# Optimization experiments

Measured on AMD Instinct MI355X. Metric: run time of the kernel, lower is better.

## Reference

```python
import jax, jax.numpy as jnp
import numpy as np

MAX_DEPTH = 11  # node positions < 2**11 = 2048


def setup_inputs() -> dict:
    key = jax.random.key(0)
    k1, k2, k3, k4, k5 = jax.random.split(key, 5)
    B, S, dim = 4, 1024, 64
    token_types = jax.random.randint(k1, (B, S), 0, 5).astype(jnp.int32)
    # token_values in [-1, 2]: -1 marks out-of-scope for scope tokens;
    # bop uses tv+1 (0..3), nop uses tv+5 (4..7) -- all in-range for the 11-row table
    token_values = (jax.random.randint(k2, (B, S), 0, 4) - 1).astype(jnp.int32)
    node_positions = jax.random.randint(k3, (B, S), 0, 2048).astype(jnp.int32)
    embed_table = jax.random.normal(k4, (11, dim), dtype=jnp.float32)
    # mirrors torch.rand(2,dim,dim).softmax(-1).cumsum(-1) init
    primitives_raw = jnp.cumsum(
        jax.nn.softmax(jax.random.uniform(k5, (2, dim, dim), dtype=jnp.float32), axis=-1),
        axis=-1)
    return {
        "token_types": token_types,
        "token_values": token_values,
        "node_positions": node_positions,
        "embed_table": embed_table,
        "primitives_raw": primitives_raw,
    }


def _forward(token_types, token_values, node_positions, embed_table, primitives_raw):
    dim = embed_table.shape[1]
    B, S = token_types.shape

    # primitives = expm(P - P^H) for each of the 2 generators
    herm = primitives_raw - jnp.swapaxes(primitives_raw, -1, -2)
    prims = jax.vmap(jax.scipy.linalg.expm)(herm)  # [2, dim, dim]

    # --- positional encodings via binary-path matrix products ---
    # path(pos) applies prims[pos%2], then prims[(pos//2)%2], ... until pos==1.
    # Equivalent to the original's per-unique-position masked-linear loop,
    # evaluated per token (== positional_encodings[inverse]).
    maps = jnp.broadcast_to(jnp.eye(dim, dtype=embed_table.dtype), (B, S, dim, dim))
    pos = node_positions
    for _ in range(MAX_DEPTH):
        active = pos > 1
        bit = (pos & 1).astype(jnp.int32)
        step_p = prims[bit]  # [B, S, dim, dim] gather of the per-step generator
        # linear(maps, prim) == maps @ prim.T, applied rowwise to each map matrix
        stepped = jnp.einsum('bsij,bskj->bsik', maps, step_p)
        maps = jnp.where(active[..., None, None], stepped, maps)
        pos = pos >> 1

    # --- content embeddings via masked gathers ---
    tt, tv = token_types, token_values
    sos = tt == 0
    bop = tt == 1
    nop = tt == 2
    scope = tt == 3
    oos = scope & (tv == -1)
    db = tt == 4
    idx = jnp.where(sos, 0,
          jnp.where(bop, tv + 1,
          jnp.where(nop, tv + 5,
          jnp.where(db, 8,
          jnp.where(oos, 10, 0)))))
    valid = sos | bop | nop | db | oos  # in-scope scope tokens stay zero
    content = jnp.where(valid[..., None], embed_table[idx], jnp.zeros((), embed_table.dtype))
    return content, maps


def reference(token_types, token_values, node_positions, embed_table, primitives_raw):
    return _forward(token_types, token_values, node_positions, embed_table, primitives_raw)
```

## Files before the change

kernel.cpp:

```cpp
#include <hip/hip_runtime.h>
#include <hip/hip_bf16.h>
#include <stdint.h>

typedef __attribute__((ext_vector_type(4))) float fx4;
typedef __attribute__((ext_vector_type(16))) float fx16;
typedef __attribute__((ext_vector_type(8))) short bx8;
typedef unsigned short u16;
typedef unsigned int u32;

#define LDW 72
#define PL (64 * LDW)
#define MAGIC 0x9E3779B9u


__device__ __forceinline__ u16 f2bf(float x) {
    u32 u = __float_as_uint(x);
    return (u16)((u + 0x7FFFu + ((u >> 16) & 1u)) >> 16);
}
__device__ __forceinline__ float bf2f(u16 h) { return __uint_as_float(((u32)h) << 16); }

__device__ __forceinline__ bx8 ld32(const u16* p, int band, int kc, int l) {
    return *(const bx8*)(p + (band * 32 + (l & 31)) * LDW + kc * 16 + (l >> 5) * 8);
}

__device__ __forceinline__ void mmG1(const u16* z1h, const u16* z1l,
                                     const u16* z2h, const u16* z2l,
                                     int ti, int tj, int l, fx16& acc) {
    fx16 ca, cb, cc;
#pragma unroll
    for (int i = 0; i < 16; ++i) { ca[i] = 0.f; cb[i] = 0.f; cc[i] = 0.f; }
#pragma unroll
    for (int kc = 0; kc < 4; ++kc) {
        bx8 ah = ld32(z1h, ti, kc, l), al = ld32(z1l, ti, kc, l);
        bx8 bh = ld32(z2h, tj, kc, l), bl = ld32(z2l, tj, kc, l);
        ca = __builtin_amdgcn_mfma_f32_32x32x16_bf16(ah, bh, ca, 0, 0, 0);
        cb = __builtin_amdgcn_mfma_f32_32x32x16_bf16(ah, bl, cb, 0, 0, 0);
        cc = __builtin_amdgcn_mfma_f32_32x32x16_bf16(al, bh, cc, 0, 0, 0);
    }
#pragma unroll
    for (int i = 0; i < 16; ++i) acc[i] = ca[i] + (cb[i] + cc[i]);
}

__device__ __forceinline__ void mmG2(const u16* z1h, const u16* z1l,
                                     const u16* z2h, const u16* z2l,
                                     int ti, int tj, int l, fx16& acc) {
    fx16 ca, cb, cc;
#pragma unroll
    for (int i = 0; i < 16; ++i) { ca[i] = 0.f; cb[i] = 0.f; cc[i] = 0.f; }
#pragma unroll
    for (int kc = 0; kc < 4; ++kc) {
        bx8 ah = ld32(z1h, ti, kc, l), al = ld32(z1l, ti, kc, l);
        bx8 bh = ld32(z2h, tj, kc, l), bl = ld32(z2l, tj, kc, l);
        ca = __builtin_amdgcn_mfma_f32_32x32x16_bf16(bh, ah, ca, 0, 0, 0);
        cb = __builtin_amdgcn_mfma_f32_32x32x16_bf16(bh, al, cb, 0, 0, 0);
        cc = __builtin_amdgcn_mfma_f32_32x32x16_bf16(bl, ah, cc, 0, 0, 0);
    }
#pragma unroll
    for (int i = 0; i < 16; ++i) acc[i] = ca[i] + (cb[i] + cc[i]);
}

__device__ __forceinline__ void stP(u16* hi, u16* lo, int TI, int TJ, int l, const fx16& a) {
    const int Ar = TJ * 32 + (l & 31);
    const int c0 = TI * 32 + 4 * (l >> 5);
#pragma unroll
    for (int q = 0; q < 4; ++q) {
        union { u16 u[4]; uint2 v; } H, L;
#pragma unroll
        for (int r = 0; r < 4; ++r) {
            float v = a[4 * q + r];
            u32 u = __float_as_uint(v);
            H.u[r] = (u16)(u >> 16);
            L.u[r] = f2bf(v - __uint_as_float(u & 0xFFFF0000u));
        }
        *(uint2*)(hi + Ar * LDW + c0 + q * 8) = H.v;
        *(uint2*)(lo + Ar * LDW + c0 + q * 8) = L.v;
    }
}

__device__ __forceinline__ void stG(u16* T, int TI, int TJ, int l, const fx16& a) {
    const int Ar = TJ * 32 + (l & 31);
    const int c0 = TI * 32 + 4 * (l >> 5);
#pragma unroll
    for (int q = 0; q < 4; ++q) {
        union { u16 u[4]; uint2 v; } pk;
#pragma unroll
        for (int r = 0; r < 4; ++r) pk.u[r] = f2bf(a[4 * q + r]);
        *(uint2*)(T + Ar * 64 + c0 + q * 8) = pk.v;
    }
}

__global__ __launch_bounds__(512) void tables_kernel(const float* __restrict__ praw,
                                                     u16* __restrict__ wsP,
                                                     u16* __restrict__ rm_bf,
                                                     u16* __restrict__ cm_bf,
                                                     u32* __restrict__ flags)
{
    __shared__ u16 S[14 * PL];
    __shared__ float Mf[64 * 65];
    const int p = blockIdx.x, tid = threadIdx.x;
    const int w = tid >> 6, l = tid & 63;
    const int wid = w & 3, half = w >> 2;
    const int ti = wid & 1, tj = wid >> 1;

    if (p < 2) {
        const int g = p;
        const float* P = praw + g * 4096;
        u16* p0h = S;            u16* p0l = S + PL;
        u16* p1h = S + 2 * PL;   u16* p1l = S + 3 * PL;
        u16* p2h = S + 4 * PL;   u16* p2l = S + 5 * PL;
        u16* p3h = S + 6 * PL;   u16* p3l = S + 7 * PL;
        float* Mf2 = (float*)(S + 8 * PL);

        const float c0c = 1.0f, c1c = 1.0f, c2c = 0.5f;
        const float c3c = 1.666666666666667e-1f, c4c = 4.166666666666667e-2f;
        const float c5c = 8.333333333333333e-3f, c6c = 1.388888888888889e-3f;
        const float c7c = 1.984126984126984e-4f, c8c = 2.48015873015873e-5f;
        const float c9c = 2.75573192239859e-6f;

        for (int s = tid; s < 4096; s += 512) {
            const int r = s >> 6, c = s & 63;
            const float m = (P[r * 64 + c] - P[c * 64 + r]) * 0.0625f;
            Mf[r * 65 + c] = m;
            u32 um = __float_as_uint(m);
            float lof = m - __uint_as_float(um & 0xFFFF0000u);
            u16 hh = (u16)(um >> 16), ll = f2bf(lof);
            p0h[r * LDW + c] = hh;  p0l[r * LDW + c] = ll;
            p1h[c * LDW + r] = hh;  p1l[c * LDW + r] = ll;
        }
        __syncthreads();

        fx16 acc, v;
        const int gcb = tj * 32 + (l & 31);
        const int r0b = ti * 32 + 4 * (l >> 5);

        if (half == 0) {
            mmG1(p1h, p1l, p0h, p0l, ti, tj, l, acc);
            stP(p2h, p2l, ti, tj, l, acc);
#pragma unroll
            for (int q = 0; q < 4; ++q)
#pragma unroll
                for (int rr = 0; rr < 4; ++rr)
                    Mf2[(r0b + q * 8 + rr) * 65 + gcb] = acc[4 * q + rr];
        }
        __syncthreads();

        if (half == 0) {
            mmG1(p2h, p2l, p0h, p0l, ti, tj, l, acc);
            stP(p3h, p3l, ti, tj, l, acc);
#pragma unroll
            for (int q = 0; q < 4; ++q)
#pragma unroll
                for (int rr = 0; rr < 4; ++rr) {
                    const int gr = r0b + q * 8 + rr;
                    v[4 * q + rr] = c9c * acc[4 * q + rr] + c8c * Mf2[gr * 65 + gcb]
                                  - c7c * Mf[gr * 65 + gcb] + (gr == gcb ? c6c : 0.f);
                }
            stP(p1h, p1l, ti, tj, l, v);
        }
        __syncthreads();

        if (half == 0) {
            mmG1(p3h, p3l, p1h, p1l, ti, tj, l, acc);
#pragma unroll
            for (int q = 0; q < 4; ++q)
#pragma unroll
                for (int rr = 0; rr < 4; ++rr) {
                    const int gr = r0b + q * 8 + rr;
                    v[4 * q + rr] = -acc[4 * q + rr] + c5c * Mf2[gr * 65 + gcb]
                                  - c4c * Mf[gr * 65 + gcb] + (gr == gcb ? c3c : 0.f);
                }
            stP(p0h, p0l, ti, tj, l, v);
        }
        __syncthreads();

        if (half == 0) {
            mmG1(p3h, p3l, p0h, p0l, ti, tj, l, acc);
#pragma unroll
            for (int q = 0; q < 4; ++q)
#pragma unroll
                for (int rr = 0; rr < 4; ++rr) {
                    const int gr = r0b + q * 8 + rr;
                    v[4 * q + rr] = -acc[4 * q + rr] + c2c * Mf2[gr * 65 + gcb]
                                  - c1c * Mf[gr * 65 + gcb] + (gr == gcb ? c0c : 0.f);
                }
            stP(p1h, p1l, ti, tj, l, v);
        } else {
            mmG1(p0h, p0l, p3h, p3l, ti, tj, l, acc);
#pragma unroll
            for (int q = 0; q < 4; ++q)
#pragma unroll
                for (int rr = 0; rr < 4; ++rr) {
                    const int gr = r0b + q * 8 + rr;
                    v[4 * q + rr] = -acc[4 * q + rr] + c2c * Mf2[gr * 65 + gcb]
                                  + c1c * Mf[gr * 65 + gcb] + (gr == gcb ? c0c : 0.f);
                }
            stP(p2h, p2l, ti, tj, l, v);
        }
        __syncthreads();

        u16 *Ych = p2h, *Ycl = p2l, *Xch = p1h, *Xcl = p1l;
        u16 *Ynh = p3h, *Ynl = p3l, *Xnh = p0h, *Xnl = p0l;
#pragma unroll 1
        for (int s4 = 0; s4 < 4; ++s4) {
            if (half == 0) {
                mmG1(Ych, Ycl, Xch, Xcl, ti, tj, l, acc);
                stP(Xnh, Xnl, ti, tj, l, acc);
            } else {
                mmG2(Ych, Ycl, Xch, Xcl, ti, tj, l, acc);
                stP(Ynh, Ynl, tj, ti, l, acc);
            }
            __syncthreads();
            u16* t;
            t = Xch; Xch = Xnh; Xnh = t;   t = Xcl; Xcl = Xnl; Xnl = t;
            t = Ych; Ych = Ynh; Ynh = t;   t = Ycl; Ycl = Ynl; Ynl = t;
        }

        {
            const int base = tid * 8, r = base >> 6, c = base & 63;
            u16* dst = wsP + g * 16384;
            *(uint4*)(dst + base)         = *(const uint4*)(Ych + r * LDW + c);
            *(uint4*)(dst + 4096 + base)  = *(const uint4*)(Ycl + r * LDW + c);
            *(uint4*)(dst + 8192 + base)  = *(const uint4*)(Xch + r * LDW + c);
            *(uint4*)(dst + 12288 + base) = *(const uint4*)(Xcl + r * LDW + c);
        }
        __threadfence();
        __syncthreads();
        if (tid < 64) atomicExch(&flags[(g * 64 + tid) * 32], MAGIC);

        for (int s = tid; s < 4096; s += 512) {
            u16 vv = ((s >> 6) == (s & 63)) ? (u16)0x3F80 : (u16)0;
            rm_bf[p * 4096 + s] = vv;
            cm_bf[p * 4096 + s] = vv;
        }
        return;
    }

    if (tid == 0) {
        while (atomicOr(&flags[(0 * 64 + p) * 32], 0u) != MAGIC) __builtin_amdgcn_s_sleep(8);
        while (atomicOr(&flags[(1 * 64 + p) * 32], 0u) != MAGIC) __builtin_amdgcn_s_sleep(8);
    }
    __syncthreads();
    __threadfence();

    const int d = 31 - __clz(p);

    if (d == 1) {
        const u16* src = wsP + (p & 1) * 16384;
        for (int s = tid; s < 4096; s += 512) {
            rm_bf[p * 4096 + s] = f2bf(bf2f(src[s]) + bf2f(src[4096 + s]));
            cm_bf[p * 4096 + s] = f2bf(bf2f(src[8192 + s]) + bf2f(src[12288 + s]));
        }
        return;
    }

    {
        const int base = tid * 8, r = base >> 6, c = base & 63;
        const int off = r * LDW + c;
        *(uint4*)(S + 0 * PL + off) = *(const uint4*)(wsP + base);
        *(uint4*)(S + 1 * PL + off) = *(const uint4*)(wsP + 4096 + base);
        *(uint4*)(S + 2 * PL + off) = *(const uint4*)(wsP + 8192 + base);
        *(uint4*)(S + 3 * PL + off) = *(const uint4*)(wsP + 12288 + base);
        *(uint4*)(S + 4 * PL + off) = *(const uint4*)(wsP + 16384 + base);
        *(uint4*)(S + 5 * PL + off) = *(const uint4*)(wsP + 16384 + 4096 + base);
        *(uint4*)(S + 6 * PL + off) = *(const uint4*)(wsP + 16384 + 8192 + base);
        *(uint4*)(S + 7 * PL + off) = *(const uint4*)(wsP + 16384 + 12288 + base);
    }
    __syncthreads();

    const int b0 = p & 1, b1 = (p >> 1) & 1, b2 = (p >> 2) & 1, b3 = (p >> 3) & 1,
              b4 = (p >> 4) & 1;
    const u16 *rm0h = S + b0 * 4 * PL,          *rm0l = rm0h + PL;
    const u16 *cm1h = S + b1 * 4 * PL + 2 * PL, *cm1l = cm1h + PL;
    const u16 *rm2h = S + b2 * 4 * PL,          *rm2l = rm2h + PL;
    const u16 *cm3h = S + b3 * 4 * PL + 2 * PL, *cm3l = cm3h + PL;
    u16 *PAh = S + 8 * PL,  *PAl = S + 9 * PL;
    u16 *PBh = S + 10 * PL, *PBl = S + 11 * PL;
    u16 *PCh = S + 12 * PL, *PCl = S + 13 * PL;

    fx16 acc;
    const u16 *fz1h, *fz1l, *fz2h, *fz2l;

    if (d == 2) {
        fz1h = cm1h; fz1l = cm1l; fz2h = rm0h; fz2l = rm0l;
    } else if (d == 3) {
        if (half == 0) {
            mmG1(cm1h, cm1l, rm0h, rm0l, ti, tj, l, acc);
            stP(PAh, PAl, ti, tj, l, acc);
        }
        __syncthreads();
        const u16* c2h = S + b2 * 4 * PL + 2 * PL;
        fz1h = c2h; fz1l = c2h + PL; fz2h = PAh; fz2l = PAl;
    } else {
        if (half == 0) {
            mmG1(cm1h, cm1l, rm0h, rm0l, ti, tj, l, acc);
            stP(PAh, PAl, ti, tj, l, acc);
        } else {
            mmG2(cm3h, cm3l, rm2h, rm2l, ti, tj, l, acc);
            stP(PBh, PBl, tj, ti, l, acc);
        }
        __syncthreads();
        if (d == 4) {
            fz1h = PBh; fz1l = PBl; fz2h = PAh; fz2l = PAl;
        } else {
            if (half == 0) {
                mmG1(PBh, PBl, PAh, PAl, ti, tj, l, acc);
                stP(PCh, PCl, ti, tj, l, acc);
            }
            __syncthreads();
            const u16* c4h = S + b4 * 4 * PL + 2 * PL;
            fz1h = c4h; fz1l = c4h + PL; fz2h = PCh; fz2l = PCl;
        }
    }

    if (half == 0) {
        mmG1(fz1h, fz1l, fz2h, fz2l, ti, tj, l, acc);
        stG(rm_bf + p * 4096, ti, tj, l, acc);
    } else {
        mmG2(fz1h, fz1l, fz2h, fz2l, ti, tj, l, acc);
        stG(cm_bf + p * 4096, tj, ti, l, acc);
    }
}

__global__ __launch_bounds__(256) void out_kernel(const int* __restrict__ tt,
                                                  const int* __restrict__ tv,
                                                  const int* __restrict__ npos,
                                                  const float* __restrict__ embed,
                                                  const u16* __restrict__ rm_bf,
                                                  const u16* __restrict__ cm_bf,
                                                  float* __restrict__ out)
{
    __shared__ float ST[4][16 * 64];
    const int tid = threadIdx.x;
    const int wv = tid >> 6, l = tid & 63;
    const int flat = blockIdx.x * 4 + wv;
    const int pos = npos[flat];

    {
        const int t = tt[flat], v = tv[flat];
        int idx; bool valid = true;
        if (t == 0)      idx = 0;
        else if (t == 1) idx = v + 1;
        else if (t == 2) idx = v + 5;
        else if (t == 4) idx = 8;
        else if (t == 3 && v == -1) idx = 10;
        else { idx = 0; valid = false; }
        out[flat * 64 + l] = valid ? embed[idx * 64 + l] : 0.f;
    }

    float* om = out + 4096 * 64 + (size_t)flat * 4096;

    if (pos < 64) {
        const u16* src = rm_bf + pos * 4096;
#pragma unroll
        for (int i = 0; i < 16; ++i) {
            const int f0 = i * 256 + l * 4;
            uint2 ld = *(const uint2*)(src + f0);
            fx4 v;
            v[0] = __uint_as_float(ld.x << 16); v[1] = __uint_as_float(ld.x & 0xFFFF0000u);
            v[2] = __uint_as_float(ld.y << 16); v[3] = __uint_as_float(ld.y & 0xFFFF0000u);
            *(fx4*)(om + f0) = v;
        }
    } else {
        const int lo5 = (pos & 31) | 32;
        const int hi5 = pos >> 5;
        const u16* Acm = cm_bf + hi5 * 4096;
        const u16* Brm = rm_bf + lo5 * 4096;
        const int lr = l & 15, h = l >> 4, k8 = h * 8;
        float* st = ST[wv];

        bx8 A0[4], A1[4], B0[4], B1[4];
#pragma unroll
        for (int q = 0; q < 4; ++q) {
            A0[q] = *(const bx8*)(Acm + (q * 16 + lr) * 64 + k8);
            A1[q] = *(const bx8*)(Acm + (q * 16 + lr) * 64 + 32 + k8);
        }
#pragma unroll
        for (int c = 0; c < 4; ++c) {
            B0[c] = *(const bx8*)(Brm + (c * 16 + lr) * 64 + k8);
            B1[c] = *(const bx8*)(Brm + (c * 16 + lr) * 64 + 32 + k8);
        }
#pragma unroll
        for (int ct = 0; ct < 4; ++ct) {
#pragma unroll
            for (int q = 0; q < 4; ++q) {
                fx4 c4 = { 0.f, 0.f, 0.f, 0.f };
                c4 = __builtin_amdgcn_mfma_f32_16x16x32_bf16(A0[q], B0[ct], c4, 0, 0, 0);
                c4 = __builtin_amdgcn_mfma_f32_16x16x32_bf16(A1[q], B1[ct], c4, 0, 0, 0);
                *(fx4*)(st + lr * 64 + 4 * ((4 * q + h) ^ lr)) = c4;
            }
#pragma unroll
            for (int i2 = 0; i2 < 4; ++i2) {
                const int row = i2 * 4 + h;
                fx4 v = *(const fx4*)(st + row * 64 + 4 * ((l & 15) ^ row));
                *(fx4*)(om + ct * 1024 + i2 * 256 + l * 4) = v;
            }
        }
    }
}

extern "C" void kernel_launch(void* const* d_in, const int* in_sizes, int n_in,
                              void* d_out, int out_size, void* d_ws, size_t ws_size,
                              hipStream_t stream)
{
    const int*   tt    = (const int*)d_in[0];
    const int*   tv    = (const int*)d_in[1];
    const int*   np    = (const int*)d_in[2];
    const float* embed = (const float*)d_in[3];
    const float* praw  = (const float*)d_in[4];
    float* out = (float*)d_out;

    u32* flags = (u32*)d_ws;
    u16* wsP   = (u16*)((char*)d_ws + 16384);
    u16* rm_bf = (u16*)((char*)d_ws + 16384 + 65536);
    u16* cm_bf = (u16*)((char*)d_ws + 16384 + 65536 + 524288);

    tables_kernel<<<dim3(64), dim3(512), 0, stream>>>(praw, wsP, rm_bf, cm_bf, flags);
    out_kernel<<<dim3(1024), dim3(256), 0, stream>>>(tt, tv, np, embed, rm_bf, cm_bf, out);
}
```

Measured before the change: 37.23 us.

## Fuse table build and output writes into one persistent kernel with per-table flags

Merges the table-construction kernel and the output kernel into a single 512-block launch. Table blocks publish per-position readiness flags, and output blocks spin on only the flags they need, so output writing can start before every table is finished. Intermediate matrices move from padded LDS to global workspace scratch, and each block now runs with 256 threads instead of 512. This removes a launch boundary and lets the two stages overlap, but adds spin-wait latency, global-memory traffic for the intermediates, and a dependence on all blocks being co-resident to avoid deadlock.

```diff
diff --git a/kernel.cpp b/kernel.cpp
--- a/kernel.cpp
+++ b/kernel.cpp
@@ -8,8 +8,6 @@
 typedef unsigned short u16;
 typedef unsigned int u32;
 
-#define LDW 72
-#define PL (64 * LDW)
 #define MAGIC 0x9E3779B9u
 
 
@@ -19,20 +17,20 @@
 }
 __device__ __forceinline__ float bf2f(u16 h) { return __uint_as_float(((u32)h) << 16); }
 
-__device__ __forceinline__ bx8 ld32(const u16* p, int band, int kc, int l) {
-    return *(const bx8*)(p + (band * 32 + (l & 31)) * LDW + kc * 16 + (l >> 5) * 8);
-}
-
-__device__ __forceinline__ void mmG1(const u16* z1h, const u16* z1l,
-                                     const u16* z2h, const u16* z2l,
-                                     int ti, int tj, int l, fx16& acc) {
+__device__ __forceinline__ bx8 gld(const u16* p, int band, int kc, int l) {
+    return *(const bx8*)(p + (band * 32 + (l & 31)) * 64 + kc * 16 + (l >> 5) * 8);
+}
+
+__device__ __forceinline__ void mmG1g(const u16* z1h, const u16* z1l,
+                                      const u16* z2h, const u16* z2l,
+                                      int ti, int tj, int l, fx16& acc) {
     fx16 ca, cb, cc;
 #pragma unroll
     for (int i = 0; i < 16; ++i) { ca[i] = 0.f; cb[i] = 0.f; cc[i] = 0.f; }
 #pragma unroll
     for (int kc = 0; kc < 4; ++kc) {
-        bx8 ah = ld32(z1h, ti, kc, l), al = ld32(z1l, ti, kc, l);
-        bx8 bh = ld32(z2h, tj, kc, l), bl = ld32(z2l, tj, kc, l);
+        bx8 ah = gld(z1h, ti, kc, l), al = gld(z1l, ti, kc, l);
+        bx8 bh = gld(z2h, tj, kc, l), bl = gld(z2l, tj, kc, l);
         ca = __builtin_amdgcn_mfma_f32_32x32x16_bf16(ah, bh, ca, 0, 0, 0);
         cb = __builtin_amdgcn_mfma_f32_32x32x16_bf16(ah, bl, cb, 0, 0, 0);
         cc = __builtin_amdgcn_mfma_f32_32x32x16_bf16(al, bh, cc, 0, 0, 0);
@@ -41,16 +39,16 @@
     for (int i = 0; i < 16; ++i) acc[i] = ca[i] + (cb[i] + cc[i]);
 }
 
-__device__ __forceinline__ void mmG2(const u16* z1h, const u16* z1l,
-                                     const u16* z2h, const u16* z2l,
-                                     int ti, int tj, int l, fx16& acc) {
+__device__ __forceinline__ void mmG2g(const u16* z1h, const u16* z1l,
+                                      const u16* z2h, const u16* z2l,
+                                      int ti, int tj, int l, fx16& acc) {
     fx16 ca, cb, cc;
 #pragma unroll
     for (int i = 0; i < 16; ++i) { ca[i] = 0.f; cb[i] = 0.f; cc[i] = 0.f; }
 #pragma unroll
     for (int kc = 0; kc < 4; ++kc) {
-        bx8 ah = ld32(z1h, ti, kc, l), al = ld32(z1l, ti, kc, l);
-        bx8 bh = ld32(z2h, tj, kc, l), bl = ld32(z2l, tj, kc, l);
+        bx8 ah = gld(z1h, ti, kc, l), al = gld(z1l, ti, kc, l);
+        bx8 bh = gld(z2h, tj, kc, l), bl = gld(z2l, tj, kc, l);
         ca = __builtin_amdgcn_mfma_f32_32x32x16_bf16(bh, ah, ca, 0, 0, 0);
         cb = __builtin_amdgcn_mfma_f32_32x32x16_bf16(bh, al, cb, 0, 0, 0);
         cc = __builtin_amdgcn_mfma_f32_32x32x16_bf16(bl, ah, cc, 0, 0, 0);
@@ -59,7 +57,7 @@
     for (int i = 0; i < 16; ++i) acc[i] = ca[i] + (cb[i] + cc[i]);
 }
 
-__device__ __forceinline__ void stP(u16* hi, u16* lo, int TI, int TJ, int l, const fx16& a) {
+__device__ __forceinline__ void stPg(u16* hi, u16* lo, int TI, int TJ, int l, const fx16& a) {
     const int Ar = TJ * 32 + (l & 31);
     const int c0 = TI * 32 + 4 * (l >> 5);
 #pragma unroll
@@ -72,8 +70,8 @@
             H.u[r] = (u16)(u >> 16);
             L.u[r] = f2bf(v - __uint_as_float(u & 0xFFFF0000u));
         }
-        *(uint2*)(hi + Ar * LDW + c0 + q * 8) = H.v;
-        *(uint2*)(lo + Ar * LDW + c0 + q * 8) = L.v;
+        *(uint2*)(hi + Ar * 64 + c0 + q * 8) = H.v;
+        *(uint2*)(lo + Ar * 64 + c0 + q * 8) = L.v;
     }
 }
 
@@ -89,251 +87,28 @@
     }
 }
 
-__global__ __launch_bounds__(512) void tables_kernel(const float* __restrict__ praw,
-                                                     u16* __restrict__ wsP,
-                                                     u16* __restrict__ rm_bf,
-                                                     u16* __restrict__ cm_bf,
-                                                     u32* __restrict__ flags)
+__device__ __forceinline__ bool waitflag(u32* f) {
+    if (atomicOr(f, 0u) == MAGIC) return false;
+    while (atomicOr(f, 0u) != MAGIC) __builtin_amdgcn_s_sleep(4);
+    return true;
+}
+
+__device__ __forceinline__ void do_token(int flat,
+        const int* __restrict__ tt, const int* __restrict__ tv,
+        const int* __restrict__ npos, const float* __restrict__ embed,
+        const u16* __restrict__ rm_bf, const u16* __restrict__ cm_bf,
+        float* __restrict__ out, u32* __restrict__ tflag, float* st, int l)
 {
-    __shared__ u16 S[14 * PL];
-    __shared__ float Mf[64 * 65];
-    const int p = blockIdx.x, tid = threadIdx.x;
-    const int w = tid >> 6, l = tid & 63;
-    const int wid = w & 3, half = w >> 2;
-    const int ti = wid & 1, tj = wid >> 1;
-
-    if (p < 2) {
-        const int g = p;
-        const float* P = praw + g * 4096;
-        u16* p0h = S;            u16* p0l = S + PL;
-        u16* p1h = S + 2 * PL;   u16* p1l = S + 3 * PL;
-        u16* p2h = S + 4 * PL;   u16* p2l = S + 5 * PL;
-        u16* p3h = S + 6 * PL;   u16* p3l = S + 7 * PL;
-        float* Mf2 = (float*)(S + 8 * PL);
-
-        const float c0c = 1.0f, c1c = 1.0f, c2c = 0.5f;
-        const float c3c = 1.666666666666667e-1f, c4c = 4.166666666666667e-2f;
-        const float c5c = 8.333333333333333e-3f, c6c = 1.388888888888889e-3f;
-        const float c7c = 1.984126984126984e-4f, c8c = 2.48015873015873e-5f;
-        const float c9c = 2.75573192239859e-6f;
-
-        for (int s = tid; s < 4096; s += 512) {
-            const int r = s >> 6, c = s & 63;
-            const float m = (P[r * 64 + c] - P[c * 64 + r]) * 0.0625f;
-            Mf[r * 65 + c] = m;
-            u32 um = __float_as_uint(m);
-            float lof = m - __uint_as_float(um & 0xFFFF0000u);
-            u16 hh = (u16)(um >> 16), ll = f2bf(lof);
-            p0h[r * LDW + c] = hh;  p0l[r * LDW + c] = ll;
-            p1h[c * LDW + r] = hh;  p1l[c * LDW + r] = ll;
-        }
-        __syncthreads();
-
-        fx16 acc, v;
-        const int gcb = tj * 32 + (l & 31);
-        const int r0b = ti * 32 + 4 * (l >> 5);
-
-        if (half == 0) {
-            mmG1(p1h, p1l, p0h, p0l, ti, tj, l, acc);
-            stP(p2h, p2l, ti, tj, l, acc);
-#pragma unroll
-            for (int q = 0; q < 4; ++q)
-#pragma unroll
-                for (int rr = 0; rr < 4; ++rr)
-                    Mf2[(r0b + q * 8 + rr) * 65 + gcb] = acc[4 * q + rr];
-        }
-        __syncthreads();
-
-        if (half == 0) {
-            mmG1(p2h, p2l, p0h, p0l, ti, tj, l, acc);
-            stP(p3h, p3l, ti, tj, l, acc);
-#pragma unroll
-            for (int q = 0; q < 4; ++q)
-#pragma unroll
-                for (int rr = 0; rr < 4; ++rr) {
-                    const int gr = r0b + q * 8 + rr;
-                    v[4 * q + rr] = c9c * acc[4 * q + rr] + c8c * Mf2[gr * 65 + gcb]
-                                  - c7c * Mf[gr * 65 + gcb] + (gr == gcb ? c6c : 0.f);
-                }
-            stP(p1h, p1l, ti, tj, l, v);
-        }
-        __syncthreads();
-
-        if (half == 0) {
-            mmG1(p3h, p3l, p1h, p1l, ti, tj, l, acc);
-#pragma unroll
-            for (int q = 0; q < 4; ++q)
-#pragma unroll
-                for (int rr = 0; rr < 4; ++rr) {
-                    const int gr = r0b + q * 8 + rr;
-                    v[4 * q + rr] = -acc[4 * q + rr] + c5c * Mf2[gr * 65 + gcb]
-                                  - c4c * Mf[gr * 65 + gcb] + (gr == gcb ? c3c : 0.f);
-                }
-            stP(p0h, p0l, ti, tj, l, v);
-        }
-        __syncthreads();
-
-        if (half == 0) {
-            mmG1(p3h, p3l, p0h, p0l, ti, tj, l, acc);
-#pragma unroll
-            for (int q = 0; q < 4; ++q)
-#pragma unroll
-                for (int rr = 0; rr < 4; ++rr) {
-                    const int gr = r0b + q * 8 + rr;
-                    v[4 * q + rr] = -acc[4 * q + rr] + c2c * Mf2[gr * 65 + gcb]
-                                  - c1c * Mf[gr * 65 + gcb] + (gr == gcb ? c0c : 0.f);
-                }
-            stP(p1h, p1l, ti, tj, l, v);
-        } else {
-            mmG1(p0h, p0l, p3h, p3l, ti, tj, l, acc);
-#pragma unroll
-            for (int q = 0; q < 4; ++q)
-#pragma unroll
-                for (int rr = 0; rr < 4; ++rr) {
-                    const int gr = r0b + q * 8 + rr;
-                    v[4 * q + rr] = -acc[4 * q + rr] + c2c * Mf2[gr * 65 + gcb]
-                                  + c1c * Mf[gr * 65 + gcb] + (gr == gcb ? c0c : 0.f);
-                }
-            stP(p2h, p2l, ti, tj, l, v);
-        }
-        __syncthreads();
-
-        u16 *Ych = p2h, *Ycl = p2l, *Xch = p1h, *Xcl = p1l;
-        u16 *Ynh = p3h, *Ynl = p3l, *Xnh = p0h, *Xnl = p0l;
-#pragma unroll 1
-        for (int s4 = 0; s4 < 4; ++s4) {
-            if (half == 0) {
-                mmG1(Ych, Ycl, Xch, Xcl, ti, tj, l, acc);
-                stP(Xnh, Xnl, ti, tj, l, acc);
-            } else {
-                mmG2(Ych, Ycl, Xch, Xcl, ti, tj, l, acc);
-                stP(Ynh, Ynl, tj, ti, l, acc);
-            }
-            __syncthreads();
-            u16* t;
-            t = Xch; Xch = Xnh; Xnh = t;   t = Xcl; Xcl = Xnl; Xnl = t;
-            t = Ych; Ych = Ynh; Ynh = t;   t = Ycl; Ycl = Ynl; Ynl = t;
-        }
-
-        {
-            const int base = tid * 8, r = base >> 6, c = base & 63;
-            u16* dst = wsP + g * 16384;
-            *(uint4*)(dst + base)         = *(const uint4*)(Ych + r * LDW + c);
-            *(uint4*)(dst + 4096 + base)  = *(const uint4*)(Ycl + r * LDW + c);
-            *(uint4*)(dst + 8192 + base)  = *(const uint4*)(Xch + r * LDW + c);
-            *(uint4*)(dst + 12288 + base) = *(const uint4*)(Xcl + r * LDW + c);
-        }
-        __threadfence();
-        __syncthreads();
-        if (tid < 64) atomicExch(&flags[(g * 64 + tid) * 32], MAGIC);
-
-        for (int s = tid; s < 4096; s += 512) {
-            u16 vv = ((s >> 6) == (s & 63)) ? (u16)0x3F80 : (u16)0;
-            rm_bf[p * 4096 + s] = vv;
-            cm_bf[p * 4096 + s] = vv;
-        }
-        return;
-    }
-
-    if (tid == 0) {
-        while (atomicOr(&flags[(0 * 64 + p) * 32], 0u) != MAGIC) __builtin_amdgcn_s_sleep(8);
-        while (atomicOr(&flags[(1 * 64 + p) * 32], 0u) != MAGIC) __builtin_amdgcn_s_sleep(8);
-    }
-    __syncthreads();
-    __threadfence();
-
-    const int d = 31 - __clz(p);
-
-    if (d == 1) {
-        const u16* src = wsP + (p & 1) * 16384;
-        for (int s = tid; s < 4096; s += 512) {
-            rm_bf[p * 4096 + s] = f2bf(bf2f(src[s]) + bf2f(src[4096 + s]));
-            cm_bf[p * 4096 + s] = f2bf(bf2f(src[8192 + s]) + bf2f(src[12288 + s]));
-        }
-        return;
-    }
-
-    {
-        const int base = tid * 8, r = base >> 6, c = base & 63;
-        const int off = r * LDW + c;
-        *(uint4*)(S + 0 * PL + off) = *(const uint4*)(wsP + base);
-        *(uint4*)(S + 1 * PL + off) = *(const uint4*)(wsP + 4096 + base);
-        *(uint4*)(S + 2 * PL + off) = *(const uint4*)(wsP + 8192 + base);
-        *(uint4*)(S + 3 * PL + off) = *(const uint4*)(wsP + 12288 + base);
-        *(uint4*)(S + 4 * PL + off) = *(const uint4*)(wsP + 16384 + base);
-        *(uint4*)(S + 5 * PL + off) = *(const uint4*)(wsP + 16384 + 4096 + base);
-        *(uint4*)(S + 6 * PL + off) = *(const uint4*)(wsP + 16384 + 8192 + base);
-        *(uint4*)(S + 7 * PL + off) = *(const uint4*)(wsP + 16384 + 12288 + base);
-    }
-    __syncthreads();
-
-    const int b0 = p & 1, b1 = (p >> 1) & 1, b2 = (p >> 2) & 1, b3 = (p >> 3) & 1,
-              b4 = (p >> 4) & 1;
-    const u16 *rm0h = S + b0 * 4 * PL,          *rm0l = rm0h + PL;
-    const u16 *cm1h = S + b1 * 4 * PL + 2 * PL, *cm1l = cm1h + PL;
-    const u16 *rm2h = S + b2 * 4 * PL,          *rm2l = rm2h + PL;
-    const u16 *cm3h = S + b3 * 4 * PL + 2 * PL, *cm3l = cm3h + PL;
-    u16 *PAh = S + 8 * PL,  *PAl = S + 9 * PL;
-    u16 *PBh = S + 10 * PL, *PBl = S + 11 * PL;
-    u16 *PCh = S + 12 * PL, *PCl = S + 13 * PL;
-
-    fx16 acc;
-    const u16 *fz1h, *fz1l, *fz2h, *fz2l;
-
-    if (d == 2) {
-        fz1h = cm1h; fz1l = cm1l; fz2h = rm0h; fz2l = rm0l;
-    } else if (d == 3) {
-        if (half == 0) {
-            mmG1(cm1h, cm1l, rm0h, rm0l, ti, tj, l, acc);
-            stP(PAh, PAl, ti, tj, l, acc);
-        }
-        __syncthreads();
-        const u16* c2h = S + b2 * 4 * PL + 2 * PL;
-        fz1h = c2h; fz1l = c2h + PL; fz2h = PAh; fz2l = PAl;
-    } else {
-        if (half == 0) {
-            mmG1(cm1h, cm1l, rm0h, rm0l, ti, tj, l, acc);
-            stP(PAh, PAl, ti, tj, l, acc);
-        } else {
-            mmG2(cm3h, cm3l, rm2h, rm2l, ti, tj, l, acc);
-            stP(PBh, PBl, tj, ti, l, acc);
-        }
-        __syncthreads();
-        if (d == 4) {
-            fz1h = PBh; fz1l = PBl; fz2h = PAh; fz2l = PAl;
-        } else {
-            if (half == 0) {
-                mmG1(PBh, PBl, PAh, PAl, ti, tj, l, acc);
-                stP(PCh, PCl, ti, tj, l, acc);
-            }
-            __syncthreads();
-            const u16* c4h = S + b4 * 4 * PL + 2 * PL;
-            fz1h = c4h; fz1l = c4h + PL; fz2h = PCh; fz2l = PCl;
-        }
-    }
-
-    if (half == 0) {
-        mmG1(fz1h, fz1l, fz2h, fz2l, ti, tj, l, acc);
-        stG(rm_bf + p * 4096, ti, tj, l, acc);
-    } else {
-        mmG2(fz1h, fz1l, fz2h, fz2l, ti, tj, l, acc);
-        stG(cm_bf + p * 4096, tj, ti, l, acc);
-    }
-}
-
-__global__ __launch_bounds__(256) void out_kernel(const int* __restrict__ tt,
-                                                  const int* __restrict__ tv,
-                                                  const int* __restrict__ npos,
-                                                  const float* __restrict__ embed,
-                                                  const u16* __restrict__ rm_bf,
-                                                  const u16* __restrict__ cm_bf,
-                                                  float* __restrict__ out)
-{
-    __shared__ float ST[4][16 * 64];
-    const int tid = threadIdx.x;
-    const int wv = tid >> 6, l = tid & 63;
-    const int flat = blockIdx.x * 4 + wv;
     const int pos = npos[flat];
+    bool w8 = false;
+    if (l == 0) {
+        if (pos < 64) w8 = waitflag(&tflag[pos * 32]);
+        else {
+            w8 = waitflag(&tflag[((pos & 31) | 32) * 32]);
+            if (waitflag(&tflag[(pos >> 5) * 32])) w8 = true;
+        }
+    }
+    if (__any(w8)) __threadfence();
 
     {
         const int t = tt[flat], v = tv[flat];
@@ -366,7 +141,6 @@
         const u16* Acm = cm_bf + hi5 * 4096;
         const u16* Brm = rm_bf + lo5 * 4096;
         const int lr = l & 15, h = l >> 4, k8 = h * 8;
-        float* st = ST[wv];
 
         bx8 A0[4], A1[4], B0[4], B1[4];
 #pragma unroll
@@ -396,6 +170,219 @@
             }
         }
     }
+}
+
+__global__ __launch_bounds__(256) void fused_kernel(
+        const int* __restrict__ tt, const int* __restrict__ tv,
+        const int* __restrict__ npos, const float* __restrict__ embed,
+        const float* __restrict__ praw, float* __restrict__ out,
+        char* __restrict__ wsbase)
+{
+    __shared__ float ST[4][1024];
+    u32* gflag = (u32*)wsbase;
+    u32* tflag = (u32*)(wsbase + 16384);
+    u16* wsP   = (u16*)(wsbase + 24576);
+    u16* rm_bf = (u16*)(wsbase + 24576 + 65536);
+    u16* cm_bf = (u16*)(wsbase + 24576 + 65536 + 524288);
+    const int b = blockIdx.x, tid = threadIdx.x;
+    const int w = tid >> 6, l = tid & 63;
+    const int ti = w & 1, tj = w >> 1;
+
+    if (b < 2) {
+        const int g = b;
+        const float* P = praw + g * 4096;
+        u16* Q = (u16*)(wsbase + 1179648 + g * 524288);
+#define QH(k) (Q + (k) * 8192)
+#define QL(k) (Q + (k) * 8192 + 4096)
+        float* Mf  = (float*)((char*)Q + 262144);
+        float* Mf2 = (float*)((char*)Q + 278528);
+
+        const float c0c = 1.0f, c1c = 1.0f, c2c = 0.5f;
+        const float c3c = 1.666666666666667e-1f, c4c = 4.166666666666667e-2f;
+        const float c5c = 8.333333333333333e-3f, c6c = 1.388888888888889e-3f;
+        const float c7c = 1.984126984126984e-4f, c8c = 2.48015873015873e-5f;
+        const float c9c = 2.75573192239859e-6f;
+
+        for (int s = tid; s < 4096; s += 256) {
+            const int r = s >> 6, c = s & 63;
+            const float m = (P[r * 64 + c] - P[c * 64 + r]) * 0.0625f;
+            Mf[s] = m;
+            u32 um = __float_as_uint(m);
+            float lof = m - __uint_as_float(um & 0xFFFF0000u);
+            u16 hh = (u16)(um >> 16), ll = f2bf(lof);
+            QH(0)[r * 64 + c] = hh;  QL(0)[r * 64 + c] = ll;
+            QH(1)[c * 64 + r] = hh;  QL(1)[c * 64 + r] = ll;
+        }
+        __threadfence(); __syncthreads();
+
+        fx16 acc, v;
+        const int gcb = tj * 32 + (l & 31);
+        const int r0b = ti * 32 + 4 * (l >> 5);
+
+        mmG1g(QH(1), QL(1), QH(0), QL(0), ti, tj, l, acc);
+        stPg(QH(2), QL(2), ti, tj, l, acc);
+#pragma unroll
+        for (int q = 0; q < 4; ++q)
+#pragma unroll
+            for (int rr = 0; rr < 4; ++rr)
+                Mf2[(r0b + q * 8 + rr) * 64 + gcb] = acc[4 * q + rr];
+        __threadfence(); __syncthreads();
+
+        mmG1g(QH(2), QL(2), QH(0), QL(0), ti, tj, l, acc);
+        stPg(QH(3), QL(3), ti, tj, l, acc);
+#pragma unroll
+        for (int q = 0; q < 4; ++q)
+#pragma unroll
+            for (int rr = 0; rr < 4; ++rr) {
+                const int gr = r0b + q * 8 + rr;
+                v[4 * q + rr] = c9c * acc[4 * q + rr] + c8c * Mf2[gr * 64 + gcb]
+                              - c7c * Mf[gr * 64 + gcb] + (gr == gcb ? c6c : 0.f);
+            }
+        stPg(QH(4), QL(4), ti, tj, l, v);
+        __threadfence(); __syncthreads();
+
+        mmG1g(QH(3), QL(3), QH(4), QL(4), ti, tj, l, acc);
+#pragma unroll
+        for (int q = 0; q < 4; ++q)
+#pragma unroll
+            for (int rr = 0; rr < 4; ++rr) {
+                const int gr = r0b + q * 8 + rr;
+                v[4 * q + rr] = -acc[4 * q + rr] + c5c * Mf2[gr * 64 + gcb]
+                              - c4c * Mf[gr * 64 + gcb] + (gr == gcb ? c3c : 0.f);
+            }
+        stPg(QH(5), QL(5), ti, tj, l, v);
+        __threadfence(); __syncthreads();
+
+        mmG1g(QH(3), QL(3), QH(5), QL(5), ti, tj, l, acc);
+#pragma unroll
+        for (int q = 0; q < 4; ++q)
+#pragma unroll
+            for (int rr = 0; rr < 4; ++rr) {
+                const int gr = r0b + q * 8 + rr;
+                v[4 * q + rr] = -acc[4 * q + rr] + c2c * Mf2[gr * 64 + gcb]
+                              - c1c * Mf[gr * 64 + gcb] + (gr == gcb ? c0c : 0.f);
+            }
+        stPg(QH(6), QL(6), ti, tj, l, v);
+        mmG1g(QH(5), QL(5), QH(3), QL(3), ti, tj, l, acc);
+#pragma unroll
+        for (int q = 0; q < 4; ++q)
+#pragma unroll
+            for (int rr = 0; rr < 4; ++rr) {
+                const int gr = r0b + q * 8 + rr;
+                v[4 * q + rr] = -acc[4 * q + rr] + c2c * Mf2[gr * 64 + gcb]
+                              + c1c * Mf[gr * 64 + gcb] + (gr == gcb ? c0c : 0.f);
+            }
+        stPg(QH(7), QL(7), ti, tj, l, v);
+        __threadfence(); __syncthreads();
+
+        const int xk[4] = {6, 8, 9, 10}, yk[4] = {7, 11, 12, 13};
+#pragma unroll 1
+        for (int s4 = 0; s4 < 4; ++s4) {
+            u16 *Yh = QH(yk[s4]), *Yl = QL(yk[s4]);
+            u16 *Xh = QH(xk[s4]), *Xl = QL(xk[s4]);
+            u16 *Xnh, *Xnl, *Ynh, *Ynl;
+            if (s4 < 3) {
+                Xnh = QH(xk[s4 + 1]); Xnl = QL(xk[s4 + 1]);
+                Ynh = QH(yk[s4 + 1]); Ynl = QL(yk[s4 + 1]);
+            } else {
+                u16* dst = wsP + g * 16384;
+                Ynh = dst;        Ynl = dst + 4096;
+                Xnh = dst + 8192; Xnl = dst + 12288;
+            }
+            mmG1g(Yh, Yl, Xh, Xl, ti, tj, l, acc);
+            stPg(Xnh, Xnl, ti, tj, l, acc);
+            mmG2g(Yh, Yl, Xh, Xl, ti, tj, l, acc);
+            stPg(Ynh, Ynl, tj, ti, l, acc);
+            __threadfence(); __syncthreads();
+        }
+#undef QH
+#undef QL
+        if (tid < 64) atomicExch(&gflag[(g * 64 + tid) * 32], MAGIC);
+
+        for (int s = tid; s < 4096; s += 256) {
+            u16 vv = ((s >> 6) == (s & 63)) ? (u16)0x3F80 : (u16)0;
+            rm_bf[g * 4096 + s] = vv;
+            cm_bf[g * 4096 + s] = vv;
+        }
+        __threadfence(); __syncthreads();
+        if (tid == 0) atomicExch(&tflag[g * 32], MAGIC);
+        return;
+    }
+
+    if (b < 64) {
+        const int p = b;
+        if (tid == 0) {
+            u32* f0 = &gflag[(0 * 64 + p) * 32];
+            while (atomicOr(f0, 0u) != MAGIC) __builtin_amdgcn_s_sleep(8);
+            u32* f1 = &gflag[(1 * 64 + p) * 32];
+            while (atomicOr(f1, 0u) != MAGIC) __builtin_amdgcn_s_sleep(8);
+        }
+        __syncthreads();
+        __threadfence();
+
+        const int d = 31 - __clz(p);
+
+        if (d == 1) {
+            const u16* src = wsP + (p & 1) * 16384;
+            for (int s = tid; s < 4096; s += 256) {
+                rm_bf[p * 4096 + s] = f2bf(bf2f(src[s]) + bf2f(src[4096 + s]));
+                cm_bf[p * 4096 + s] = f2bf(bf2f(src[8192 + s]) + bf2f(src[12288 + s]));
+            }
+        } else {
+            const int b0 = p & 1, b1 = (p >> 1) & 1, b2 = (p >> 2) & 1,
+                      b3 = (p >> 3) & 1, b4 = (p >> 4) & 1;
+            const u16 *rm0h = wsP + b0 * 16384,        *rm0l = rm0h + 4096;
+            const u16 *cm1h = wsP + b1 * 16384 + 8192, *cm1l = cm1h + 4096;
+            const u16 *rm2h = wsP + b2 * 16384,        *rm2l = rm2h + 4096;
+            const u16 *cm3h = wsP + b3 * 16384 + 8192, *cm3l = cm3h + 4096;
+            u16* CB = (u16*)(wsbase + 2228224 + (size_t)p * 65536);
+            u16 *PAh = CB,         *PAl = CB + 4096;
+            u16 *PBh = CB + 8192,  *PBl = CB + 12288;
+            u16 *PCh = CB + 16384, *PCl = CB + 20480;
+
+            fx16 acc;
+            const u16 *fz1h, *fz1l, *fz2h, *fz2l;
+
+            if (d == 2) {
+                fz1h = cm1h; fz1l = cm1l; fz2h = rm0h; fz2l = rm0l;
+            } else if (d == 3) {
+                mmG1g(cm1h, cm1l, rm0h, rm0l, ti, tj, l, acc);
+                stPg(PAh, PAl, ti, tj, l, acc);
+                __threadfence(); __syncthreads();
+                const u16* c2h = wsP + b2 * 16384 + 8192;
+                fz1h = c2h; fz1l = c2h + 4096; fz2h = PAh; fz2l = PAl;
+            } else {
+                mmG1g(cm1h, cm1l, rm0h, rm0l, ti, tj, l, acc);
+                stPg(PAh, PAl, ti, tj, l, acc);
+                mmG2g(cm3h, cm3l, rm2h, rm2l, ti, tj, l, acc);
+                stPg(PBh, PBl, tj, ti, l, acc);
+                __threadfence(); __syncthreads();
+                if (d == 4) {
+                    fz1h = PBh; fz1l = PBl; fz2h = PAh; fz2l = PAl;
+                } else {
+                    mmG1g(PBh, PBl, PAh, PAl, ti, tj, l, acc);
+                    stPg(PCh, PCl, ti, tj, l, acc);
+                    __threadfence(); __syncthreads();
+                    const u16* c4h = wsP + b4 * 16384 + 8192;
+                    fz1h = c4h; fz1l = c4h + 4096; fz2h = PCh; fz2l = PCl;
+                }
+            }
+            mmG1g(fz1h, fz1l, fz2h, fz2l, ti, tj, l, acc);
+            stG(rm_bf + p * 4096, ti, tj, l, acc);
+            mmG2g(fz1h, fz1l, fz2h, fz2l, ti, tj, l, acc);
+            stG(cm_bf + p * 4096, tj, ti, l, acc);
+        }
+        __threadfence(); __syncthreads();
+        if (tid == 0) atomicExch(&tflag[p * 32], MAGIC);
+        return;
+    }
+
+    int nt, t0;
+    if (b < 128) { nt = 10; t0 = (b - 64) * 10; }
+    else         { nt = 9;  t0 = 640 + (b - 128) * 9; }
+#pragma unroll 1
+    for (int k = w; k < nt; k += 4)
+        do_token(t0 + k, tt, tv, npos, embed, rm_bf, cm_bf, out, tflag, ST[w], l);
 }
 
 extern "C" void kernel_launch(void* const* d_in, const int* in_sizes, int n_in,
@@ -409,11 +396,6 @@
     const float* praw  = (const float*)d_in[4];
     float* out = (float*)d_out;
 
-    u32* flags = (u32*)d_ws;
-    u16* wsP   = (u16*)((char*)d_ws + 16384);
-    u16* rm_bf = (u16*)((char*)d_ws + 16384 + 65536);
-    u16* cm_bf = (u16*)((char*)d_ws + 16384 + 65536 + 524288);
-
-    tables_kernel<<<dim3(64), dim3(512), 0, stream>>>(praw, wsP, rm_bf, cm_bf, flags);
-    out_kernel<<<dim3(1024), dim3(256), 0, stream>>>(tt, tv, np, embed, rm_bf, cm_bf, out);
-}
+    fused_kernel<<<dim3(512), dim3(256), 0, stream>>>(tt, tv, np, embed, praw, out,
+                                                      (char*)d_ws);
+}
```

Measured after the change: 103.6 us. 2.78x slower.
